# Kernel tuning notes

Hardware: AMD Instinct MI355X
Metric: run time of the kernel (lower is better)

## Reference

```python
import jax, jax.numpy as jnp
import numpy as np

EPS = 1e-5
RANGES = (1, 2)           # max_range per scale; min_range (radius) = 0
CIN, CMID, COUT = 64, 32, 64
N_PTS, M_GRID = 16384, 65536
B, Z, Y, X = 2, 11, 200, 176


def make_offsets(r):
    # replicates TorchGrouper.index_offset: cat(arange(-r,-0), arange(0,r)) per dim,
    # z varies slowest, x fastest; channel 0 is the batch offset (=0)
    rt = jnp.arange(-r, r)
    z, y, x = jnp.meshgrid(rt, rt, rt, indexing='ij')
    return jnp.stack([jnp.zeros_like(x), x, y, z], axis=-1).reshape(-1, 4)  # (K,4)


def bn(v, gamma, beta):
    # train-mode BatchNorm over the row axis (channels last), biased variance, eps=1e-5
    mu = v.mean(0, keepdims=True)
    var = v.var(0, keepdims=True)
    return (v - mu) * jax.lax.rsqrt(var + EPS) * gamma + beta


def setup_inputs() -> dict:
    key = jax.random.key(0)
    ks = jax.random.split(key, 16)
    xyz = jax.random.normal(ks[0], (N_PTS, 3), jnp.float32)
    new_xyz = jax.random.normal(ks[1], (M_GRID, 3), jnp.float32)
    features = jax.random.normal(ks[2], (N_PTS, CIN), jnp.float32)
    xyz_batch_cnt = jnp.array([N_PTS // 2, N_PTS - N_PTS // 2], jnp.int32)
    new_xyz_batch_cnt = jnp.array([M_GRID // 2, M_GRID - M_GRID // 2], jnp.int32)
    # new_coords columns: [b, x, y, z] (forward permutes to [b, z, y, x])
    bcol = jax.random.randint(ks[3], (M_GRID,), 0, B, jnp.int32)
    xcol = jax.random.randint(ks[4], (M_GRID,), 0, X, jnp.int32)
    ycol = jax.random.randint(ks[5], (M_GRID,), 0, Y, jnp.int32)
    zcol = jax.random.randint(ks[6], (M_GRID,), 0, Z, jnp.int32)
    new_coords = jnp.stack([bcol, xcol, ycol, zcol], axis=1)
    # voxel map: point index per voxel, -1 = empty
    voxel2point_indices = jax.random.randint(ks[7], (B, Z, Y, X), -1, N_PTS, jnp.int32)
    s_in = np.sqrt(2.0 / CIN).astype(np.float32)
    s_pos = np.sqrt(2.0 / 3.0).astype(np.float32)
    s_out = np.sqrt(2.0 / CMID).astype(np.float32)
    return {
        'xyz': xyz, 'xyz_batch_cnt': xyz_batch_cnt,
        'new_xyz': new_xyz, 'new_xyz_batch_cnt': new_xyz_batch_cnt,
        'new_coords': new_coords, 'features': features,
        'voxel2point_indices': voxel2point_indices,
        'W_in': jax.random.normal(ks[8], (2, CMID, CIN), jnp.float32) * s_in,
        'g_in': jnp.ones((2, CMID), jnp.float32), 'b_in': jnp.zeros((2, CMID), jnp.float32),
        'W_pos': jax.random.normal(ks[9], (2, CMID, 3), jnp.float32) * s_pos,
        'g_pos': jnp.ones((2, CMID), jnp.float32), 'b_pos': jnp.zeros((2, CMID), jnp.float32),
        'W_out': jax.random.normal(ks[10], (2, COUT, CMID), jnp.float32) * s_out,
        'g_out': jnp.ones((2, COUT), jnp.float32), 'b_out': jnp.zeros((2, COUT), jnp.float32),
    }


def reference(xyz, xyz_batch_cnt, new_xyz, new_xyz_batch_cnt, new_coords, features,
              voxel2point_indices, W_in, g_in, b_in, W_pos, g_pos, b_pos,
              W_out, g_out, b_out):
    vm = voxel2point_indices
    _, Zd, Yd, Xd = vm.shape
    nc = new_coords[:, jnp.array([0, 3, 2, 1])]          # (M,4) -> b,z,y,x
    outs = []
    for k, r in enumerate(RANGES):
        off = make_offsets(r)                             # (K,4) int
        # mlps_in: Conv1d(1x1) + BN over all N points
        f = bn(features @ W_in[k].T, g_in[k], b_in[k])    # (N,Cm)
        f_pad = jnp.concatenate([jnp.zeros((1, CMID), f.dtype), f], axis=0)
        pos = nc[:, None, :] + off[None]                  # (M,K,4)
        bi = pos[..., 0]
        zi = jnp.clip(pos[..., 1], 0, Zd - 1)
        yi = jnp.clip(pos[..., 2], 0, Yd - 1)
        xi = jnp.clip(pos[..., 3], 0, Xd - 1)
        idx = vm[bi, zi, yi, xi]                          # (M,K) gather, -1 -> pad row
        gf = f_pad[idx + 1]                               # (M,K,Cm)
        # mlps_pos: grid positions are integers so (p - floor(p)) == 0; the position
        # feature is exactly the integer offset vector, constant across M, so the
        # train-mode BN stats over (M,K) reduce to stats over K.
        pf = bn(off[:, 1:4].astype(f.dtype) @ W_pos[k].T, g_pos[k], b_pos[k])  # (K,Cm)
        nf = jax.nn.relu(gf + pf[None]).max(axis=1)       # max-pool over K -> (M,Cm)
        o = jax.nn.relu(bn(nf @ W_out[k].T, g_out[k], b_out[k]))               # (M,Cout)
        outs.append(o)
    return jnp.concatenate(outs, axis=1)                  # (M, 2*Cout)
```

## Files before the change

### kernel.cpp

```cpp
#include <hip/hip_runtime.h>

#define EPSV 1e-5f
constexpr int NPTS  = 16384;
constexpr int MGRID = 65536;
constexpr int ZD = 11, YD = 200, XD = 176;
constexpr int NVOX = 2 * ZD * YD * XD;
constexpr int NB_VM = (NVOX / 8 + 255) / 256;

typedef _Float16 h2  __attribute__((ext_vector_type(2)));
typedef _Float16 h8v __attribute__((ext_vector_type(8)));
struct alignas(16) H8 { h2 a, b, c, d; };

#if __has_builtin(__builtin_amdgcn_fdot2)
#define FDOT2(a, b, c) __builtin_amdgcn_fdot2((a), (b), (c), false)
#else
#define FDOT2(a, b, c) ((c) + (float)(a).x * (float)(b).x + (float)(a).y * (float)(b).y)
#endif


__device__ __forceinline__ h8v gload_h8(const _Float16* p) {
    h8v r;
    asm volatile("global_load_dwordx4 %0, %1, off" : "=v"(r) : "v"(p));
    return r;
}
__device__ __forceinline__ uint4 gload_u128(const void* p) {
    uint4 r;
    asm volatile("global_load_dwordx4 %0, %1, off" : "=v"(r) : "v"(p));
    return r;
}
__device__ __forceinline__ uint2 gload_u64(const void* p) {
    uint2 r;
    asm volatile("global_load_dwordx2 %0, %1, off" : "=v"(r) : "v"(p));
    return r;
}
__device__ __forceinline__ void vm_wait0() {
    asm volatile("s_waitcnt vmcnt(0)" ::: "memory");
    __builtin_amdgcn_sched_barrier(0);
}
__device__ __forceinline__ h8v zero8() {
    h8v z;
#pragma unroll
    for (int i = 0; i < 8; ++i) z[i] = (_Float16)0.f;
    return z;
}
__device__ __forceinline__ h8v shfl_xor_h8(h8v v, int m) {
    union { h8v h; int4 i; } u; u.h = v;
    u.i.x = __shfl_xor(u.i.x, m, 64);
    u.i.y = __shfl_xor(u.i.y, m, 64);
    u.i.z = __shfl_xor(u.i.z, m, 64);
    u.i.w = __shfl_xor(u.i.w, m, 64);
    return u.h;
}

__global__ __launch_bounds__(256) void k_pre(
    const int* __restrict__ vm, const float* __restrict__ features,
    const float* __restrict__ Win, const float* __restrict__ Wpos,
    const float* __restrict__ g_pos, const float* __restrict__ b_pos,
    short* __restrict__ vm16, _Float16* __restrict__ fraw_h,
    float* __restrict__ pIn, float* __restrict__ pf)
{
    __shared__ float smem[2688];
    int bid = blockIdx.x, t = threadIdx.x;

    if (bid < NB_VM) {
        int i = bid * 256 + t;
        if (i < NVOX / 8) {
            int4 v0 = ((const int4*)vm)[i * 2];
            int4 v1 = ((const int4*)vm)[i * 2 + 1];
            uint4 o;
            o.x = (v0.x & 0xffff) | (v0.y << 16);
            o.y = (v0.z & 0xffff) | (v0.w << 16);
            o.z = (v1.x & 0xffff) | (v1.y << 16);
            o.w = (v1.z & 0xffff) | (v1.w << 16);
            ((uint4*)vm16)[i] = o;
        }
        return;
    }
    if (bid < NB_VM + 512) {
        int b2 = bid - NB_VM;
        int k = b2 >> 8, bx = b2 & 255;
        float* Wls = smem;
        float* s_  = smem + 2176;
        float* q_  = smem + 2432;
        for (int idx = t; idx < 2048; idx += 256)
            Wls[(idx >> 6) * 68 + (idx & 63)] = Win[k * 2048 + idx];
        __syncthreads();
        int c = t & 31, g = t >> 5;
        float w[64];
#pragma unroll
        for (int i4 = 0; i4 < 16; ++i4) {
            float4 wv = *(const float4*)&Wls[c * 68 + i4 * 4];
            w[i4 * 4] = wv.x; w[i4 * 4 + 1] = wv.y; w[i4 * 4 + 2] = wv.z; w[i4 * 4 + 3] = wv.w;
        }
        int base = bx * 64;
        float ssum = 0.f, ssq = 0.f;
        for (int it = 0; it < 8; ++it) {
            int pt = base + it * 8 + g;
            const float4* fr = (const float4*)(features + (size_t)pt * 64);
            float y = 0.f;
#pragma unroll
            for (int i4 = 0; i4 < 16; ++i4) {
                float4 v = fr[i4];
                y += v.x * w[i4 * 4] + v.y * w[i4 * 4 + 1] + v.z * w[i4 * 4 + 2] + v.w * w[i4 * 4 + 3];
            }
            fraw_h[((size_t)k * (NPTS + 1) + pt + 1) * 32 + c] = (_Float16)y;
            ssum += y; ssq += y * y;
        }
        s_[t] = ssum; q_[t] = ssq;
        __syncthreads();
        if (t < 32) {
            float fs = 0.f, fq = 0.f;
#pragma unroll
            for (int gg = 0; gg < 8; ++gg) { fs += s_[gg * 32 + t]; fq += q_[gg * 32 + t]; }
            float* pb = pIn + ((size_t)k * 256 + bx) * 64;
            pb[t] = fs; pb[32 + t] = fq;
        }
        return;
    }
    float* praw = smem;
    int pfoff = 0;
    for (int k = 0; k < 2; ++k) {
        int r = k + 1, s = 2 * r, noff = s * s * s;
        for (int idx = t; idx < noff * 32; idx += 256) {
            int j = idx >> 5, c = idx & 31;
            int xi = j % s, yi = (j / s) % s, zi = j / (s * s);
            const float* W = Wpos + (k * 32 + c) * 3;
            praw[idx] = (float)(xi - r) * W[0] + (float)(yi - r) * W[1] + (float)(zi - r) * W[2];
        }
        __syncthreads();
        if (t < 32) {
            float sum = 0.f, sq = 0.f;
            for (int j = 0; j < noff; ++j) { float v = praw[j * 32 + t]; sum += v; sq += v * v; }
            float mu  = sum / (float)noff;
            float var = fmaxf(sq / (float)noff - mu * mu, 0.f);
            float rs  = rsqrtf(var + EPSV);
            float g = g_pos[k * 32 + t], b = b_pos[k * 32 + t];
            for (int j = 0; j < noff; ++j)
                pf[pfoff + j * 32 + t] = (praw[j * 32 + t] - mu) * rs * g + b;
        }
        __syncthreads();
        pfoff += noff * 32;
    }
}

__global__ __launch_bounds__(256) void k_reduce_in(
    const float* __restrict__ pIn, const float* __restrict__ g_in,
    const float* __restrict__ b_in, float* __restrict__ ss_in,
    _Float16* __restrict__ fraw_h)
{
    __shared__ float ss[256], qq[256];
    int b = blockIdx.x;
    int k = b >> 5, c = b & 31;
    int t = threadIdx.x;
    ss[t] = pIn[((size_t)k * 256 + t) * 64 + c];
    qq[t] = pIn[((size_t)k * 256 + t) * 64 + 32 + c];
    __syncthreads();
    if (t < 128) { ss[t] += ss[t + 128]; qq[t] += qq[t + 128]; } __syncthreads();
    if (t < 64)  { ss[t] += ss[t + 64];  qq[t] += qq[t + 64];  } __syncthreads();
    if (t < 32)  { ss[t] += ss[t + 32];  qq[t] += qq[t + 32];  } __syncthreads();
    if (t == 0) {
        float sv = 0.f, sq = 0.f;
#pragma unroll
        for (int i = 0; i < 32; ++i) { sv += ss[i]; sq += qq[i]; }
        float mu  = sv / (float)NPTS;
        float var = fmaxf(sq / (float)NPTS - mu * mu, 0.f);
        float rs  = rsqrtf(var + EPSV);
        float scale = g_in[k * 32 + c] * rs;
        float shift = b_in[k * 32 + c] - mu * scale;
        ss_in[k * 64 + c]      = scale;
        ss_in[k * 64 + 32 + c] = shift;
        float pad = (scale != 0.f) ? (-shift / scale) : 0.f;
        pad = fminf(fmaxf(pad, -60000.f), 60000.f);
        fraw_h[(size_t)k * (NPTS + 1) * 32 + c] = (_Float16)pad;
    }
}

__global__ __launch_bounds__(256) void k_gather(
    const int* __restrict__ nc, const short* __restrict__ vm16,
    const _Float16* __restrict__ fraw_h, const float* __restrict__ pf,
    const float* __restrict__ ss_in, _Float16* __restrict__ nf_h)
{
    __shared__ __align__(16) _Float16 psum1[64 * 40];
    __shared__ __align__(16) _Float16 psum0[8 * 40];
    int t = threadIdx.x, bx = blockIdx.x;
    int c4 = t & 3, jg = (t >> 2) & 3, lp = t >> 4;
    int pt = bx * 16 + lp;

    int4 cc = ((const int4*)nc)[pt];
    int bb = cc.x, xc = cc.y, yc = cc.z, zc = cc.w;
    int Zo[4];
#pragma unroll
    for (int u = 0; u < 4; ++u) {
        int zq = min(max(zc + u - 2, 0), ZD - 1);
        Zo[u] = (bb * ZD + zq) * (YD * XD);
    }
    int Yo1 = min(max(yc + jg - 2, 0), YD - 1) * XD;
    int ax1 = (min(max(xc - 2, 0), XD - 4)) & ~1;
    int Xoff[4];
#pragma unroll
    for (int a = 0; a < 4; ++a)
        Xoff[a] = min(max(xc - 2 + a, 0), XD - 1) - ax1;
    int zq0 = min(max(zc + (jg & 1) - 1, 0), ZD - 1);
    int yo0 = min(max(yc + (jg >> 1) - 1, 0), YD - 1) * XD;
    int zo0 = (bb * ZD + zq0) * (YD * XD);
    int x0a = min(max(xc - 1, 0), XD - 1);
    int x0b = min(max(xc, 0), XD - 1);
    int ax0 = x0a & ~1;
    int X0a = x0a - ax0, X0b = x0b - ax0;
    __builtin_amdgcn_sched_barrier(0);

    uint4 pk[4];
#pragma unroll
    for (int u = 0; u < 4; ++u)
        pk[u] = gload_u128(vm16 + Zo[u] + Yo1 + ax1);
    uint2 pk0 = gload_u64(vm16 + zo0 + yo0 + ax0);

    for (int i = t; i < 2048; i += 256) {
        int o = i >> 5, ch = i & 31;
        psum1[o * 40 + ch] = (_Float16)(pf[256 + i] + ss_in[96 + ch]);
    }
    {
        int o = t >> 5, ch = t & 31;
        psum0[o * 40 + ch] = (_Float16)(pf[t] + ss_in[32 + ch]);
    }
    __syncthreads();
    vm_wait0();

    const _Float16* fr1 = fraw_h + (size_t)(NPTS + 1) * 32;
    h8v g1[16], g0[2];
#pragma unroll
    for (int u = 0; u < 4; ++u) {
        unsigned long long lo = (unsigned long long)pk[u].x | ((unsigned long long)pk[u].y << 32);
        unsigned long long hi = (unsigned long long)pk[u].z | ((unsigned long long)pk[u].w << 32);
#pragma unroll
        for (int a = 0; a < 4; ++a) {
            int off = Xoff[a];
            unsigned long long sel = (off & 4) ? hi : lo;
            unsigned row = ((unsigned)(sel >> ((off & 3) * 16)) + 1) & 0xFFFFu;
            g1[u * 4 + a] = gload_h8(fr1 + (size_t)row * 32 + c4 * 8);
        }
    }
    {
        unsigned long long l0 = (unsigned long long)pk0.x | ((unsigned long long)pk0.y << 32);
        unsigned r0 = ((unsigned)(l0 >> (X0a * 16)) + 1) & 0xFFFFu;
        unsigned r1 = ((unsigned)(l0 >> (X0b * 16)) + 1) & 0xFFFFu;
        g0[0] = gload_h8(fraw_h + (size_t)r0 * 32 + c4 * 8);
        g0[1] = gload_h8(fraw_h + (size_t)r1 * 32 + c4 * 8);
    }
    vm_wait0();

    h8v sc1v, sc0v;
#pragma unroll
    for (int i = 0; i < 8; ++i) {
        sc1v[i] = (_Float16)ss_in[64 + c4 * 8 + i];
        sc0v[i] = (_Float16)ss_in[c4 * 8 + i];
    }
    h8v acc1 = zero8(), acc0 = zero8();
#pragma unroll
    for (int i = 0; i < 16; ++i) {
        int o = (i & 3) * 16 + jg * 4 + (i >> 2);
        h8v pv = *(const h8v*)(psum1 + o * 40 + c4 * 8);
        acc1 = __builtin_elementwise_max(acc1, g1[i] * sc1v + pv);
    }
    {
        h8v pv = *(const h8v*)(psum0 + jg * 40 + c4 * 8);
        acc0 = __builtin_elementwise_max(acc0, g0[0] * sc0v + pv);
        h8v pv2 = *(const h8v*)(psum0 + (4 + jg) * 40 + c4 * 8);
        acc0 = __builtin_elementwise_max(acc0, g0[1] * sc0v + pv2);
    }
    acc1 = __builtin_elementwise_max(acc1, shfl_xor_h8(acc1, 4));
    acc1 = __builtin_elementwise_max(acc1, shfl_xor_h8(acc1, 8));
    acc0 = __builtin_elementwise_max(acc0, shfl_xor_h8(acc0, 4));
    acc0 = __builtin_elementwise_max(acc0, shfl_xor_h8(acc0, 8));
    if (jg == 0) {
        *(h8v*)(nf_h + ((size_t)MGRID + pt) * 32 + c4 * 8) = acc1;
        *(h8v*)(nf_h + (size_t)pt * 32 + c4 * 8) = acc0;
    }
}

__global__ __launch_bounds__(256) void k_out_stats(
    const _Float16* __restrict__ nf_h, const float* __restrict__ Wout,
    float* __restrict__ pOut)
{
    __shared__ __align__(16) _Float16 nfs[128 * 32];
    __shared__ h2 Wh[64 * 17];
    __shared__ float s_[256], q_[256];
    int k = blockIdx.y, t = threadIdx.x, bx = blockIdx.x;
    const _Float16* src = nf_h + ((size_t)k * MGRID + (size_t)bx * 128) * 32;
    ((uint4*)nfs)[t]       = ((const uint4*)src)[t];
    ((uint4*)nfs)[256 + t] = ((const uint4*)src)[256 + t];
    for (int i = t; i < 1024; i += 256) {
        int c = i >> 4, q = i & 15;
        h2 v;
        v.x = (_Float16)Wout[k * 2048 + c * 32 + 2 * q];
        v.y = (_Float16)Wout[k * 2048 + c * 32 + 2 * q + 1];
        Wh[c * 17 + q] = v;
    }
    __syncthreads();
    int c = t & 63, pg = t >> 6;
    h2 w[16];
#pragma unroll
    for (int i = 0; i < 16; ++i) w[i] = Wh[c * 17 + i];
    float sum = 0.f, sq = 0.f;
    for (int i = 0; i < 32; ++i) {
        const h2* row = (const h2*)(nfs + (pg * 32 + i) * 32);
        float y = 0.f;
#pragma unroll
        for (int iq = 0; iq < 16; ++iq) y = FDOT2(row[iq], w[iq], y);
        sum += y; sq += y * y;
    }
    s_[t] = sum; q_[t] = sq;
    __syncthreads();
    if (t < 128) { s_[t] += s_[t + 128]; q_[t] += q_[t + 128]; }
    __syncthreads();
    if (t < 64) {
        pOut[((size_t)k * 512 + bx) * 128 + t]      = s_[t] + s_[t + 64];
        pOut[((size_t)k * 512 + bx) * 128 + 64 + t] = q_[t] + q_[t + 64];
    }
}

__global__ __launch_bounds__(256) void k_out_reduce(
    const float* __restrict__ pOut, const float* __restrict__ g_out,
    const float* __restrict__ b_out, float* __restrict__ ss_out)
{
    __shared__ float ss[256], qq[256];
    int b = blockIdx.x;
    int k = b >> 6, c = b & 63;
    int t = threadIdx.x;
    float sv = 0.f, sq = 0.f;
#pragma unroll
    for (int i = 0; i < 2; ++i) {
        size_t row = (size_t)k * 512 + t + i * 256;
        sv += pOut[row * 128 + c];
        sq += pOut[row * 128 + 64 + c];
    }
    ss[t] = sv; qq[t] = sq;
    __syncthreads();
    if (t < 128) { ss[t] += ss[t + 128]; qq[t] += qq[t + 128]; } __syncthreads();
    if (t < 64)  { ss[t] += ss[t + 64];  qq[t] += qq[t + 64];  } __syncthreads();
    if (t < 32)  { ss[t] += ss[t + 32];  qq[t] += qq[t + 32];  } __syncthreads();
    if (t == 0) {
        float fs = 0.f, fq = 0.f;
#pragma unroll
        for (int i = 0; i < 32; ++i) { fs += ss[i]; fq += qq[i]; }
        float mu  = fs / (float)MGRID;
        float var = fmaxf(fq / (float)MGRID - mu * mu, 0.f);
        float rs  = rsqrtf(var + EPSV);
        float scale = g_out[k * 64 + c] * rs;
        float shift = b_out[k * 64 + c] - mu * scale;
        ss_out[k * 128 + c]      = scale;
        ss_out[k * 128 + 64 + c] = shift;
    }
}

__global__ __launch_bounds__(256) void k_out_write(
    const _Float16* __restrict__ nf_h, const float* __restrict__ Wout,
    const float* __restrict__ ss_out, float* __restrict__ out)
{
    __shared__ h2 Wh[64 * 17];
    int k = blockIdx.y, t = threadIdx.x;
    for (int i = t; i < 1024; i += 256) {
        int c = i >> 4, q = i & 15;
        h2 v;
        v.x = (_Float16)Wout[k * 2048 + c * 32 + 2 * q];
        v.y = (_Float16)Wout[k * 2048 + c * 32 + 2 * q + 1];
        Wh[c * 17 + q] = v;
    }
    __syncthreads();
    int c = t & 63, pl = t >> 6;
    float scale = ss_out[k * 128 + c], shift = ss_out[k * 128 + 64 + c];
    const h2* w = &Wh[c * 17];
    int base = blockIdx.x * 64;
    for (int it = 0; it < 16; ++it) {
        int pt = base + it * 4 + pl;
        const H8* row = (const H8*)(nf_h + ((size_t)k * MGRID + pt) * 32);
        H8 r0 = row[0], r1 = row[1], r2 = row[2], r3 = row[3];
        h2 hh[16] = {r0.a, r0.b, r0.c, r0.d, r1.a, r1.b, r1.c, r1.d,
                     r2.a, r2.b, r2.c, r2.d, r3.a, r3.b, r3.c, r3.d};
        float y = 0.f;
#pragma unroll
        for (int iq = 0; iq < 16; ++iq) y = FDOT2(hh[iq], w[iq], y);
        float o = y * scale + shift;
        out[(size_t)pt * 128 + k * 64 + c] = o > 0.f ? o : 0.f;
    }
}

extern "C" void kernel_launch(void* const* d_in, const int* in_sizes, int n_in,
                              void* d_out, int out_size, void* d_ws, size_t ws_size,
                              hipStream_t stream) {
    const int*   new_coords = (const int*)d_in[4];
    const float* features   = (const float*)d_in[5];
    const int*   vm         = (const int*)d_in[6];
    const float* W_in  = (const float*)d_in[7];
    const float* g_in  = (const float*)d_in[8];
    const float* b_in  = (const float*)d_in[9];
    const float* W_pos = (const float*)d_in[10];
    const float* g_pos = (const float*)d_in[11];
    const float* b_pos = (const float*)d_in[12];
    const float* W_out = (const float*)d_in[13];
    const float* g_out = (const float*)d_in[14];
    const float* b_out = (const float*)d_in[15];
    float* out = (float*)d_out;

    char* ws = (char*)d_ws;
    float*     ss_in  = (float*)(ws);
    float*     ss_out = (float*)(ws + 4096);
    float*     pIn    = (float*)(ws + 8192);
    _Float16*  fraw_h = (_Float16*)(ws + 139264);
    float*     pf     = (float*)(ws + 2236544);
    short*     vm16   = (short*)(ws + 2245760);
    _Float16*  nf_h   = (_Float16*)(ws + 3794560);
    float*     pOut   = (float*)(ws + 12183168);

    k_pre<<<NB_VM + 512 + 1, 256, 0, stream>>>(vm, features, W_in, W_pos, g_pos, b_pos,
                                               vm16, fraw_h, pIn, pf);
    k_reduce_in<<<64, 256, 0, stream>>>(pIn, g_in, b_in, ss_in, fraw_h);

    k_gather<<<MGRID / 16, 256, 0, stream>>>(new_coords, vm16, fraw_h, pf, ss_in, nf_h);

    dim3 gS(512, 2);
    k_out_stats<<<gS, 256, 0, stream>>>(nf_h, W_out, pOut);

    k_out_reduce<<<128, 256, 0, stream>>>(pOut, g_out, b_out, ss_out);

    dim3 gW(MGRID / 64, 2);
    k_out_write<<<gW, 256, 0, stream>>>(nf_h, W_out, ss_out, out);
}
```

Before: 89.83 us.

## Precompute fp16 position-bias tables once and reuse range-2 voxel rows for range-1

The fp32 position-feature-plus-shift tables that every gather block rebuilt in shared memory (followed by a barrier) are now built once in fp16 by the BN reduction kernel and read from global memory in the gather. The gather no longer issues its own voxel-map load for the range-1 scale. It takes the needed voxel indices from the range-2 rows already loaded by neighbouring lanes via cross-lane shuffles. This removes per-block table construction, one barrier and one global load, at the cost of extra shuffles and global/L1 reads of the table inside the max loop.

```diff
diff --git a/kernel.cpp b/kernel.cpp
--- a/kernel.cpp
+++ b/kernel.cpp
@@ -26,11 +26,6 @@
 __device__ __forceinline__ uint4 gload_u128(const void* p) {
     uint4 r;
     asm volatile("global_load_dwordx4 %0, %1, off" : "=v"(r) : "v"(p));
-    return r;
-}
-__device__ __forceinline__ uint2 gload_u64(const void* p) {
-    uint2 r;
-    asm volatile("global_load_dwordx2 %0, %1, off" : "=v"(r) : "v"(p));
     return r;
 }
 __device__ __forceinline__ void vm_wait0() {
@@ -145,10 +140,12 @@
 
 __global__ __launch_bounds__(256) void k_reduce_in(
     const float* __restrict__ pIn, const float* __restrict__ g_in,
-    const float* __restrict__ b_in, float* __restrict__ ss_in,
-    _Float16* __restrict__ fraw_h)
+    const float* __restrict__ b_in, const float* __restrict__ pf,
+    float* __restrict__ ss_in, _Float16* __restrict__ fraw_h,
+    _Float16* __restrict__ psum0_h, _Float16* __restrict__ psum1_h)
 {
     __shared__ float ss[256], qq[256];
+    __shared__ float sh_shift;
     int b = blockIdx.x;
     int k = b >> 5, c = b & 31;
     int t = threadIdx.x;
@@ -172,16 +169,23 @@
         float pad = (scale != 0.f) ? (-shift / scale) : 0.f;
         pad = fminf(fmaxf(pad, -60000.f), 60000.f);
         fraw_h[(size_t)k * (NPTS + 1) * 32 + c] = (_Float16)pad;
+        sh_shift = shift;
+    }
+    __syncthreads();
+    float shift = sh_shift;
+    if (k == 1) {
+        if (t < 64) psum1_h[t * 32 + c] = (_Float16)(pf[256 + t * 32 + c] + shift);
+    } else {
+        if (t < 8)  psum0_h[t * 32 + c] = (_Float16)(pf[t * 32 + c] + shift);
     }
 }
 
 __global__ __launch_bounds__(256) void k_gather(
     const int* __restrict__ nc, const short* __restrict__ vm16,
-    const _Float16* __restrict__ fraw_h, const float* __restrict__ pf,
+    const _Float16* __restrict__ fraw_h,
+    const _Float16* __restrict__ psum0_h, const _Float16* __restrict__ psum1_h,
     const float* __restrict__ ss_in, _Float16* __restrict__ nf_h)
 {
-    __shared__ __align__(16) _Float16 psum1[64 * 40];
-    __shared__ __align__(16) _Float16 psum0[8 * 40];
     int t = threadIdx.x, bx = blockIdx.x;
     int c4 = t & 3, jg = (t >> 2) & 3, lp = t >> 4;
     int pt = bx * 16 + lp;
@@ -200,31 +204,27 @@
 #pragma unroll
     for (int a = 0; a < 4; ++a)
         Xoff[a] = min(max(xc - 2 + a, 0), XD - 1) - ax1;
-    int zq0 = min(max(zc + (jg & 1) - 1, 0), ZD - 1);
-    int yo0 = min(max(yc + (jg >> 1) - 1, 0), YD - 1) * XD;
-    int zo0 = (bb * ZD + zq0) * (YD * XD);
     int x0a = min(max(xc - 1, 0), XD - 1);
     int x0b = min(max(xc, 0), XD - 1);
-    int ax0 = x0a & ~1;
-    int X0a = x0a - ax0, X0b = x0b - ax0;
+    int pos0a = x0a - ax1, pos0b = x0b - ax1;
     __builtin_amdgcn_sched_barrier(0);
 
     uint4 pk[4];
 #pragma unroll
     for (int u = 0; u < 4; ++u)
         pk[u] = gload_u128(vm16 + Zo[u] + Yo1 + ax1);
-    uint2 pk0 = gload_u64(vm16 + zo0 + yo0 + ax0);
-
-    for (int i = t; i < 2048; i += 256) {
-        int o = i >> 5, ch = i & 31;
-        psum1[o * 40 + ch] = (_Float16)(pf[256 + i] + ss_in[96 + ch]);
-    }
-    {
-        int o = t >> 5, ch = t & 31;
-        psum0[o * 40 + ch] = (_Float16)(pf[t] + ss_in[32 + ch]);
-    }
-    __syncthreads();
     vm_wait0();
+
+    int sl = ((t & 63) & ~12) | ((((jg >> 1) & 1) + 1) << 2);
+    int p1x = __shfl((int)pk[1].x, sl, 64);
+    int p1y = __shfl((int)pk[1].y, sl, 64);
+    int p2x = __shfl((int)pk[2].x, sl, 64);
+    int p2y = __shfl((int)pk[2].y, sl, 64);
+    unsigned long long sel64 = (jg & 1)
+        ? ((unsigned long long)(unsigned)p2x | ((unsigned long long)(unsigned)p2y << 32))
+        : ((unsigned long long)(unsigned)p1x | ((unsigned long long)(unsigned)p1y << 32));
+    unsigned r0 = ((unsigned)(sel64 >> (pos0a * 16)) + 1) & 0xFFFFu;
+    unsigned r1 = ((unsigned)(sel64 >> (pos0b * 16)) + 1) & 0xFFFFu;
 
     const _Float16* fr1 = fraw_h + (size_t)(NPTS + 1) * 32;
     h8v g1[16], g0[2];
@@ -240,13 +240,8 @@
             g1[u * 4 + a] = gload_h8(fr1 + (size_t)row * 32 + c4 * 8);
         }
     }
-    {
-        unsigned long long l0 = (unsigned long long)pk0.x | ((unsigned long long)pk0.y << 32);
-        unsigned r0 = ((unsigned)(l0 >> (X0a * 16)) + 1) & 0xFFFFu;
-        unsigned r1 = ((unsigned)(l0 >> (X0b * 16)) + 1) & 0xFFFFu;
-        g0[0] = gload_h8(fraw_h + (size_t)r0 * 32 + c4 * 8);
-        g0[1] = gload_h8(fraw_h + (size_t)r1 * 32 + c4 * 8);
-    }
+    g0[0] = gload_h8(fraw_h + (size_t)r0 * 32 + c4 * 8);
+    g0[1] = gload_h8(fraw_h + (size_t)r1 * 32 + c4 * 8);
     vm_wait0();
 
     h8v sc1v, sc0v;
@@ -259,13 +254,13 @@
 #pragma unroll
     for (int i = 0; i < 16; ++i) {
         int o = (i & 3) * 16 + jg * 4 + (i >> 2);
-        h8v pv = *(const h8v*)(psum1 + o * 40 + c4 * 8);
+        h8v pv = *(const h8v*)(psum1_h + o * 32 + c4 * 8);
         acc1 = __builtin_elementwise_max(acc1, g1[i] * sc1v + pv);
     }
     {
-        h8v pv = *(const h8v*)(psum0 + jg * 40 + c4 * 8);
+        h8v pv = *(const h8v*)(psum0_h + jg * 32 + c4 * 8);
         acc0 = __builtin_elementwise_max(acc0, g0[0] * sc0v + pv);
-        h8v pv2 = *(const h8v*)(psum0 + (4 + jg) * 40 + c4 * 8);
+        h8v pv2 = *(const h8v*)(psum0_h + (4 + jg) * 32 + c4 * 8);
         acc0 = __builtin_elementwise_max(acc0, g0[1] * sc0v + pv2);
     }
     acc1 = __builtin_elementwise_max(acc1, shfl_xor_h8(acc1, 4));
@@ -403,20 +398,24 @@
     float* out = (float*)d_out;
 
     char* ws = (char*)d_ws;
-    float*     ss_in  = (float*)(ws);
-    float*     ss_out = (float*)(ws + 4096);
-    float*     pIn    = (float*)(ws + 8192);
-    _Float16*  fraw_h = (_Float16*)(ws + 139264);
-    float*     pf     = (float*)(ws + 2236544);
-    short*     vm16   = (short*)(ws + 2245760);
-    _Float16*  nf_h   = (_Float16*)(ws + 3794560);
-    float*     pOut   = (float*)(ws + 12183168);
+    float*     ss_in   = (float*)(ws);
+    float*     ss_out  = (float*)(ws + 4096);
+    float*     pIn     = (float*)(ws + 8192);
+    _Float16*  fraw_h  = (_Float16*)(ws + 139264);
+    float*     pf      = (float*)(ws + 2236544);
+    short*     vm16    = (short*)(ws + 2245760);
+    _Float16*  nf_h    = (_Float16*)(ws + 3794560);
+    float*     pOut    = (float*)(ws + 12183168);
+    _Float16*  psum0_h = (_Float16*)(ws + 12707840);
+    _Float16*  psum1_h = (_Float16*)(ws + 12708352);
 
     k_pre<<<NB_VM + 512 + 1, 256, 0, stream>>>(vm, features, W_in, W_pos, g_pos, b_pos,
                                                vm16, fraw_h, pIn, pf);
-    k_reduce_in<<<64, 256, 0, stream>>>(pIn, g_in, b_in, ss_in, fraw_h);
-
-    k_gather<<<MGRID / 16, 256, 0, stream>>>(new_coords, vm16, fraw_h, pf, ss_in, nf_h);
+    k_reduce_in<<<64, 256, 0, stream>>>(pIn, g_in, b_in, pf, ss_in, fraw_h,
+                                        psum0_h, psum1_h);
+
+    k_gather<<<MGRID / 16, 256, 0, stream>>>(new_coords, vm16, fraw_h,
+                                             psum0_h, psum1_h, ss_in, nf_h);
 
     dim3 gS(512, 2);
     k_out_stats<<<gS, 256, 0, stream>>>(nf_h, W_out, pOut);
```

Result: slower. 92.55 us (+3.0%).
